# Kernel optimization log

Measured on AMD Instinct MI355X. Metric: run time of the kernel, lower is better.

The kernel has to match this reference:

```python
import jax, jax.numpy as jnp
import numpy as np

M, N, DIM, B = 64, 64, 512, 4096
SIGMA = max(M, N) / 2.0  # default sigma in BaseSOM.__init__


def setup_inputs() -> dict:
    key = jax.random.key(0)
    k1, k2 = jax.random.split(key)
    batch = jax.random.normal(k1, (B, DIM), dtype=jnp.float32)
    weights = jax.random.uniform(k2, (M * N, DIM), dtype=jnp.float32)
    # grid locations [(i, j) for i in range(M) for j in range(N)]
    ii, jj = jnp.meshgrid(jnp.arange(M), jnp.arange(N), indexing="ij")
    locations = jnp.stack([ii.reshape(-1), jj.reshape(-1)], axis=1).astype(jnp.int64)
    return {
        "batch": batch,
        "weights": weights,
        "locations": locations,
        "decay_rate": 1000,
        "it": 100,
    }


def reference(batch, weights, locations, decay_rate, it):
    # Squared Euclidean distances (argmin is identical to argmin of cdist p=2).
    x2 = jnp.sum(batch * batch, axis=1, keepdims=True)          # [B, 1]
    w2 = jnp.sum(weights * weights, axis=1)[None, :]            # [1, MN]
    d2 = x2 - 2.0 * (batch @ weights.T) + w2                    # [B, MN]
    bmu_indices = jnp.argmin(d2, axis=1)                        # [B]
    bmu_loc = locations[bmu_indices]                            # [B, 2]
    lr = jnp.exp(-jnp.float32(it) / jnp.float32(decay_rate))
    sigma_op = jnp.float32(SIGMA) * lr
    # [B, MN, 2] grid offsets -> squared grid distance [B, MN]
    diff = locations[None, :, :].astype(jnp.float32) - bmu_loc[:, None, :].astype(jnp.float32)
    dist_sq = jnp.sum(diff * diff, axis=2)
    return jnp.exp(-dist_sq / (sigma_op * sigma_op))
```

## Files before the change

### kernel.cpp

```cpp
#include <hip/hip_runtime.h>
#include <cfloat>

#define DIMK 512
#define MN   4096
#define BATCH 4096
#define BK 32
#define NGRP 1024

typedef _Float16 half8_t __attribute__((ext_vector_type(8)));
typedef float f32x4 __attribute__((ext_vector_type(4)));

#define GLD16(gp, lp) __builtin_amdgcn_global_load_lds( \
    (const __attribute__((address_space(1))) void*)(gp), \
    (__attribute__((address_space(3))) void*)(lp), 16, 0, 0)

__global__ __launch_bounds__(256) void convert_kernel(
        const float* __restrict__ X, const float* __restrict__ W,
        _Float16* __restrict__ Xh, _Float16* __restrict__ Wh,
        float* __restrict__ w2, float* __restrict__ xnorm) {
    const int blk  = blockIdx.x;
    const int t    = threadIdx.x;
    const bool isW = blk >= 1024;
    const float* src = isW ? W : X;
    _Float16* dst  = isW ? Wh : Xh;
    const int rblk = isW ? blk - 1024 : blk;
    const size_t idx = (size_t)rblk * 2048 + (size_t)t * 8;

    float4 v0 = *(const float4*)(src + idx);
    float4 v1 = *(const float4*)(src + idx + 4);
    float v[8] = {v0.x, v0.y, v0.z, v0.w, v1.x, v1.y, v1.z, v1.w};
    half8_t hv;
    float s = 0.f;
#pragma unroll
    for (int e = 0; e < 8; e++) {
        s += v[e] * v[e];
        hv[e] = (_Float16)v[e];
    }
    *(half8_t*)(dst + idx) = hv;
#pragma unroll
    for (int o = 32; o > 0; o >>= 1) s += __shfl_down(s, o);
    if ((t & 63) == 0) {
        int row = rblk * 4 + (t >> 6);
        if (isW) w2[row] = s;
        else     xnorm[row] = __fsqrt_rn(s);
    }
}

__global__ __launch_bounds__(256, 4) void score_kernel(
        const _Float16* __restrict__ Xh, const _Float16* __restrict__ Wh,
        const float* __restrict__ w2, float* __restrict__ Gm ) {
    __shared__ __align__(16) _Float16 lds[2][8192];

    const int t    = threadIdx.x;
    const int lane = t & 63;
    const int w    = t >> 6;
    const int wm   = w >> 1;
    const int wn   = w & 1;
    const int m0   = blockIdx.y * 128;
    const int n0   = blockIdx.x * 128;

    f32x4 acc[4][4];
#pragma unroll
    for (int i = 0; i < 4; i++)
#pragma unroll
        for (int j = 0; j < 4; j++) acc[i][j] = (f32x4){0.f, 0.f, 0.f, 0.f};

    const int r16 = lane & 15;
    const int kg  = lane >> 4;
    const int b0  = 2 * w, b1 = 2 * w + 1;
    const size_t ko = (size_t)kg * 8;
    const _Float16* gA0 = Xh + (size_t)(m0 + b0 * 16 + r16) * DIMK + ko;
    const _Float16* gA1 = Xh + (size_t)(m0 + b1 * 16 + r16) * DIMK + ko;
    const _Float16* gB0 = Wh + (size_t)(n0 + b0 * 16 + r16) * DIMK + ko;
    const _Float16* gB1 = Wh + (size_t)(n0 + b1 * 16 + r16) * DIMK + ko;
    const int dA0 = b0 * 512,        dA1 = b1 * 512;
    const int dB0 = 4096 + b0 * 512, dB1 = 4096 + b1 * 512;

    GLD16(gA0, &lds[0][dA0]);
    GLD16(gA1, &lds[0][dA1]);
    GLD16(gB0, &lds[0][dB0]);
    GLD16(gB1, &lds[0][dB1]);

    int cur = 0;
    for (int k0 = 0; k0 < DIMK; k0 += BK) {
        __syncthreads();
        if (k0 + BK < DIMK) {
            int nk = k0 + BK;
            GLD16(gA0 + nk, &lds[cur ^ 1][dA0]);
            GLD16(gA1 + nk, &lds[cur ^ 1][dA1]);
            GLD16(gB0 + nk, &lds[cur ^ 1][dB0]);
            GLD16(gB1 + nk, &lds[cur ^ 1][dB1]);
        }
        const _Float16* sA = &lds[cur][0];
        const _Float16* sB = &lds[cur][4096];

        half8_t ah[4], bh[4];
#pragma unroll
        for (int i = 0; i < 4; i++) {
            ah[i] = *(const half8_t*)(sA + (wm * 4 + i) * 512 + lane * 8);
            bh[i] = *(const half8_t*)(sB + (wn * 4 + i) * 512 + lane * 8);
        }
#pragma unroll
        for (int i = 0; i < 4; i++)
#pragma unroll
            for (int j = 0; j < 4; j++)
                acc[i][j] = __builtin_amdgcn_mfma_f32_16x16x32_f16(ah[i], bh[j], acc[i][j], 0, 0, 0);
        cur ^= 1;
    }

    const int q   = lane >> 4;
    const int cl  = lane & 15;
    const int gb  = (n0 >> 2) + wn * 16;
    float w2v[4];
#pragma unroll
    for (int j = 0; j < 4; j++) w2v[j] = w2[n0 + wn * 64 + j * 16 + cl];
#pragma unroll
    for (int i = 0; i < 4; i++)
#pragma unroll
        for (int v = 0; v < 4; v++) {
            const int row = m0 + wm * 64 + i * 16 + q * 4 + v;
            float* grow = Gm + (size_t)row * 4096 + gb;
#pragma unroll
            for (int j = 0; j < 4; j++) {
                float s = w2v[j] - 2.0f * acc[i][j][v];
                s = fminf(s, __shfl_xor(s, 1));
                s = fminf(s, __shfl_xor(s, 2));
                if ((cl & 3) == 0) grow[j * 4 + (cl >> 2)] = s;
            }
        }
}

__global__ __launch_bounds__(256) void epilogue_kernel(
        const float* __restrict__ w2, const float* __restrict__ xnorm,
        const float* __restrict__ X, const float* __restrict__ W,
        const int* __restrict__ decay_p, const int* __restrict__ it_p,
        float* out) {
    __shared__ float xs[512];
    __shared__ int   list[NGRP];
    __shared__ int   cnt;
    __shared__ float wmin[4];
    __shared__ float svv[4];
    __shared__ int   svi[4];
    __shared__ float sbv;
    __shared__ int   sbi;
    __shared__ float tab[128];
    const int row  = blockIdx.x;
    const int t    = threadIdx.x;
    const int lane = t & 63;
    const int w    = t >> 6;

    {
        float2 xv = *(const float2*)(X + (size_t)row * DIMK + t * 2);
        xs[2 * t]     = xv.x;
        xs[2 * t + 1] = xv.y;
    }
    if (t == 0) { cnt = 0; sbv = FLT_MAX; sbi = 0x7FFFFFFF; }

    f32x4 gm = *((const f32x4*)(out + (size_t)row * 4096) + t);
    float g = fminf(fminf(gm[0], gm[1]), fminf(gm[2], gm[3]));
#pragma unroll
    for (int mask = 1; mask <= 32; mask <<= 1)
        g = fminf(g, __shfl_xor(g, mask));
    if (lane == 0) wmin[w] = g;
    __syncthreads();
    const float gmin = fminf(fminf(wmin[0], wmin[1]), fminf(wmin[2], wmin[3]));
    const float tau  = gmin + 2.0f * (0.0222f * xnorm[row] + 0.1f);

#pragma unroll
    for (int e = 0; e < 4; e++)
        if (gm[e] <= tau) list[atomicAdd(&cnt, 1)] = t * 4 + e;
    __syncthreads();
    const int total = cnt;

    for (int idx = 0; idx < total; idx++) {
        const int col = list[idx] * 4 + w;
        const float* wr = W + (size_t)col * DIMK;
        float p = 0.f;
#pragma unroll
        for (int e = 0; e < 8; e++) p += xs[lane * 8 + e] * wr[lane * 8 + e];
#pragma unroll
        for (int mask = 1; mask <= 32; mask <<= 1) p += __shfl_xor(p, mask);
        if (lane == 0) {
            svv[w] = w2[col] - 2.0f * p;
            svi[w] = col;
        }
        __syncthreads();
        if (t == 0) {
#pragma unroll
            for (int k = 0; k < 4; k++) {
                float s = svv[k]; int c = svi[k];
                if (s < sbv || (s == sbv && c < sbi)) { sbv = s; sbi = c; }
            }
        }
        __syncthreads();
    }

    const float lr  = __expf(-(float)(*it_p) / (float)(*decay_p));
    const float so  = 32.0f * lr;
    const float inv = 1.0f / (so * so);
    const int rr = sbi >> 6, cc = sbi & 63;
    if (t < 64) {
        float d = (float)(t - rr);
        tab[t] = __expf(-d * d * inv);
    } else if (t < 128) {
        float d = (float)(t - 64 - cc);
        tab[t] = __expf(-d * d * inv);
    }
    __syncthreads();
    const float* er = tab;
    const float* ec = tab + 64;
    f32x4* orow = (f32x4*)(out + (size_t)row * 4096);
#pragma unroll
    for (int qq = 0; qq < 4; qq++) {
        int f  = qq * 256 + t;
        int i  = f >> 4;
        int j0 = (f & 15) * 4;
        float e = er[i];
        f32x4 o = {e * ec[j0], e * ec[j0 + 1], e * ec[j0 + 2], e * ec[j0 + 3]};
        __builtin_nontemporal_store(o, orow + f);
    }
}

extern "C" void kernel_launch(void* const* d_in, const int* in_sizes, int n_in,
                              void* d_out, int out_size, void* d_ws, size_t ws_size,
                              hipStream_t stream) {
    const float* X       = (const float*)d_in[0];
    const float* W       = (const float*)d_in[1];
    const int*   decay_p = (const int*)d_in[3];
    const int*   it_p    = (const int*)d_in[4];
    float* out = (float*)d_out;

    _Float16* Xh = (_Float16*)d_ws;
    _Float16* Wh = Xh + (size_t)BATCH * DIMK;
    float*    w2 = (float*)(Wh + (size_t)MN * DIMK);
    float*    xn = w2 + MN;

    convert_kernel<<<2048, 256, 0, stream>>>(X, W, Xh, Wh, w2, xn);
    score_kernel<<<dim3(32, 32), 256, 0, stream>>>(Xh, Wh, w2, out);
    epilogue_kernel<<<BATCH, 256, 0, stream>>>(w2, xn, X, W, decay_p, it_p, out);
}
```

Before: 144.8 us.

## Load A fragments directly from global into registers, stage only B in LDS

The X (A-operand) tile now goes straight from global memory into registers, with a one-step register prefetch. Only the W (B-operand) tile is still staged through LDS with double buffering, which halves LDS usage and LDS traffic per block. In exchange, each pair of waves sharing a row group reloads the same A data from global/L2, so global reads of X double. More registers are live for the prefetched fragments.

```diff
diff --git a/kernel.cpp b/kernel.cpp
--- a/kernel.cpp
+++ b/kernel.cpp
@@ -49,7 +49,7 @@
 __global__ __launch_bounds__(256, 4) void score_kernel(
         const _Float16* __restrict__ Xh, const _Float16* __restrict__ Wh,
         const float* __restrict__ w2, float* __restrict__ Gm ) {
-    __shared__ __align__(16) _Float16 lds[2][8192];
+    __shared__ __align__(16) _Float16 lds[2][4096];
 
     const int t    = threadIdx.x;
     const int lane = t & 63;
@@ -67,44 +67,48 @@
 
     const int r16 = lane & 15;
     const int kg  = lane >> 4;
-    const int b0  = 2 * w, b1 = 2 * w + 1;
     const size_t ko = (size_t)kg * 8;
-    const _Float16* gA0 = Xh + (size_t)(m0 + b0 * 16 + r16) * DIMK + ko;
-    const _Float16* gA1 = Xh + (size_t)(m0 + b1 * 16 + r16) * DIMK + ko;
+
+    const int b0 = 2 * w, b1 = 2 * w + 1;
     const _Float16* gB0 = Wh + (size_t)(n0 + b0 * 16 + r16) * DIMK + ko;
     const _Float16* gB1 = Wh + (size_t)(n0 + b1 * 16 + r16) * DIMK + ko;
-    const int dA0 = b0 * 512,        dA1 = b1 * 512;
-    const int dB0 = 4096 + b0 * 512, dB1 = 4096 + b1 * 512;
-
-    GLD16(gA0, &lds[0][dA0]);
-    GLD16(gA1, &lds[0][dA1]);
+    const int dB0 = b0 * 512, dB1 = b1 * 512;
+
+    const _Float16* gA[4];
+#pragma unroll
+    for (int i = 0; i < 4; i++)
+        gA[i] = Xh + (size_t)(m0 + wm * 64 + i * 16 + r16) * DIMK + ko;
+
     GLD16(gB0, &lds[0][dB0]);
     GLD16(gB1, &lds[0][dB1]);
+    half8_t ac[4];
+#pragma unroll
+    for (int i = 0; i < 4; i++) ac[i] = *(const half8_t*)(gA[i]);
 
     int cur = 0;
     for (int k0 = 0; k0 < DIMK; k0 += BK) {
         __syncthreads();
-        if (k0 + BK < DIMK) {
-            int nk = k0 + BK;
-            GLD16(gA0 + nk, &lds[cur ^ 1][dA0]);
-            GLD16(gA1 + nk, &lds[cur ^ 1][dA1]);
+        const bool more = (k0 + BK) < DIMK;
+        const int  nk   = more ? (k0 + BK) : 0;
+        if (more) {
             GLD16(gB0 + nk, &lds[cur ^ 1][dB0]);
             GLD16(gB1 + nk, &lds[cur ^ 1][dB1]);
         }
-        const _Float16* sA = &lds[cur][0];
-        const _Float16* sB = &lds[cur][4096];
-
-        half8_t ah[4], bh[4];
-#pragma unroll
-        for (int i = 0; i < 4; i++) {
-            ah[i] = *(const half8_t*)(sA + (wm * 4 + i) * 512 + lane * 8);
-            bh[i] = *(const half8_t*)(sB + (wn * 4 + i) * 512 + lane * 8);
-        }
+        half8_t an[4];
+#pragma unroll
+        for (int i = 0; i < 4; i++) an[i] = *(const half8_t*)(gA[i] + nk);
+        const _Float16* sB = &lds[cur][0];
+        half8_t bh[4];
+#pragma unroll
+        for (int j = 0; j < 4; j++)
+            bh[j] = *(const half8_t*)(sB + (wn * 4 + j) * 512 + lane * 8);
 #pragma unroll
         for (int i = 0; i < 4; i++)
 #pragma unroll
             for (int j = 0; j < 4; j++)
-                acc[i][j] = __builtin_amdgcn_mfma_f32_16x16x32_f16(ah[i], bh[j], acc[i][j], 0, 0, 0);
+                acc[i][j] = __builtin_amdgcn_mfma_f32_16x16x32_f16(ac[i], bh[j], acc[i][j], 0, 0, 0);
+#pragma unroll
+        for (int i = 0; i < 4; i++) ac[i] = an[i];
         cur ^= 1;
     }
 
```

Measured after the change: 158.9 us. +9.7%, slower.

## Store group-min scores as fp16 and parallelize candidate rescoring across warps

Applied to the files above, without the earlier changes.

The score kernel now writes its per-group minimum scores to the output buffer as fp16 instead of fp32, halving that intermediate write and the epilogue's reread. The candidate tolerance is widened to absorb the extra fp16 rounding error. The epilogue's candidate loop is restructured so each warp takes whole candidate groups and tracks its own best locally, replacing two block barriers per candidate with a single final reduction. The wider threshold can add candidates and so more exact fp32 dot products per row.

```diff
diff --git a/kernel.cpp b/kernel.cpp
--- a/kernel.cpp
+++ b/kernel.cpp
@@ -8,6 +8,7 @@
 #define NGRP 1024
 
 typedef _Float16 half8_t __attribute__((ext_vector_type(8)));
+typedef _Float16 half4_t __attribute__((ext_vector_type(4)));
 typedef float f32x4 __attribute__((ext_vector_type(4)));
 
 #define GLD16(gp, lp) __builtin_amdgcn_global_load_lds( \
@@ -119,13 +120,13 @@
 #pragma unroll
         for (int v = 0; v < 4; v++) {
             const int row = m0 + wm * 64 + i * 16 + q * 4 + v;
-            float* grow = Gm + (size_t)row * 4096 + gb;
+            _Float16* grow = (_Float16*)Gm + (size_t)row * 8192 + gb;
 #pragma unroll
             for (int j = 0; j < 4; j++) {
                 float s = w2v[j] - 2.0f * acc[i][j][v];
                 s = fminf(s, __shfl_xor(s, 1));
                 s = fminf(s, __shfl_xor(s, 2));
-                if ((cl & 3) == 0) grow[j * 4 + (cl >> 2)] = s;
+                if ((cl & 3) == 0) grow[j * 4 + (cl >> 2)] = (_Float16)s;
             }
         }
 }
@@ -141,8 +142,6 @@
     __shared__ float wmin[4];
     __shared__ float svv[4];
     __shared__ int   svi[4];
-    __shared__ float sbv;
-    __shared__ int   sbi;
     __shared__ float tab[128];
     const int row  = blockIdx.x;
     const int t    = threadIdx.x;
@@ -154,45 +153,49 @@
         xs[2 * t]     = xv.x;
         xs[2 * t + 1] = xv.y;
     }
-    if (t == 0) { cnt = 0; sbv = FLT_MAX; sbi = 0x7FFFFFFF; }
-
-    f32x4 gm = *((const f32x4*)(out + (size_t)row * 4096) + t);
-    float g = fminf(fminf(gm[0], gm[1]), fminf(gm[2], gm[3]));
+    if (t == 0) cnt = 0;
+
+    half4_t gmh = *((const half4_t*)((const _Float16*)out + (size_t)row * 8192) + t);
+    float gme[4] = {(float)gmh[0], (float)gmh[1], (float)gmh[2], (float)gmh[3]};
+    float g = fminf(fminf(gme[0], gme[1]), fminf(gme[2], gme[3]));
 #pragma unroll
     for (int mask = 1; mask <= 32; mask <<= 1)
         g = fminf(g, __shfl_xor(g, mask));
     if (lane == 0) wmin[w] = g;
     __syncthreads();
     const float gmin = fminf(fminf(wmin[0], wmin[1]), fminf(wmin[2], wmin[3]));
-    const float tau  = gmin + 2.0f * (0.0222f * xnorm[row] + 0.1f);
+    const float tau  = gmin + 2.0f * (0.0222f * xnorm[row] + 0.25f);
 
 #pragma unroll
     for (int e = 0; e < 4; e++)
-        if (gm[e] <= tau) list[atomicAdd(&cnt, 1)] = t * 4 + e;
+        if (gme[e] <= tau) list[atomicAdd(&cnt, 1)] = t * 4 + e;
     __syncthreads();
     const int total = cnt;
 
-    for (int idx = 0; idx < total; idx++) {
-        const int col = list[idx] * 4 + w;
-        const float* wr = W + (size_t)col * DIMK;
-        float p = 0.f;
-#pragma unroll
-        for (int e = 0; e < 8; e++) p += xs[lane * 8 + e] * wr[lane * 8 + e];
-#pragma unroll
-        for (int mask = 1; mask <= 32; mask <<= 1) p += __shfl_xor(p, mask);
-        if (lane == 0) {
-            svv[w] = w2[col] - 2.0f * p;
-            svi[w] = col;
-        }
-        __syncthreads();
-        if (t == 0) {
-#pragma unroll
-            for (int k = 0; k < 4; k++) {
-                float s = svv[k]; int c = svi[k];
-                if (s < sbv || (s == sbv && c < sbi)) { sbv = s; sbi = c; }
-            }
-        }
-        __syncthreads();
+    float mbv = FLT_MAX;
+    int   mbi = 0x7FFFFFFF;
+    for (int idx = w; idx < total; idx += 4) {
+        const int gid = list[idx];
+#pragma unroll
+        for (int cj = 0; cj < 4; cj++) {
+            const int col = gid * 4 + cj;
+            const float* wr = W + (size_t)col * DIMK;
+            float p = 0.f;
+#pragma unroll
+            for (int e = 0; e < 8; e++) p += xs[lane * 8 + e] * wr[lane * 8 + e];
+#pragma unroll
+            for (int mask = 1; mask <= 32; mask <<= 1) p += __shfl_xor(p, mask);
+            float s = w2[col] - 2.0f * p;
+            if (s < mbv || (s == mbv && col < mbi)) { mbv = s; mbi = col; }
+        }
+    }
+    if (lane == 0) { svv[w] = mbv; svi[w] = mbi; }
+    __syncthreads();
+    float sbv = svv[0]; int sbi = svi[0];
+#pragma unroll
+    for (int k = 1; k < 4; k++) {
+        float s = svv[k]; int c = svi[k];
+        if (s < sbv || (s == sbv && c < sbi)) { sbv = s; sbi = c; }
     }
 
     const float lr  = __expf(-(float)(*it_p) / (float)(*decay_p));
```

After: 144.2 us. About the same (-0.4%).
